# Kernel tuning notes

Hardware: AMD Instinct MI355X
Metric: run time of the kernel (lower is better)

## Reference

```python
import jax, jax.numpy as jnp
import numpy as np

H = 1024    # hidden_size
E = 1024    # embedding_size
V = 50257   # vocab_size
M = 16384   # current number of entity slots in h_e_m


def setup_inputs() -> dict:
    key = jax.random.key(0)
    ks = jax.random.split(key, 12)
    u = lambda k, s: jax.random.uniform(k, s, jnp.float32, -0.1, 0.1)
    return dict(
        x=jax.random.randint(ks[0], (1,), 0, V),
        entity_target=jax.random.randint(ks[1], (1,), 1, M),
        emb=u(ks[2], (V, E)),
        W_ih=u(ks[3], (4 * H, E)),
        W_hh=u(ks[4], (4 * H, H)),
        b_ih=jnp.zeros((4 * H,), jnp.float32),
        b_hh=jnp.zeros((4 * H,), jnp.float32),
        h0=jnp.zeros((1, H), jnp.float32),
        c0=jnp.zeros((1, H), jnp.float32),
        h_e_m=u(ks[5], (M, H)),
        Ws_w=u(ks[6], (H, H)),
        Ws_b=jnp.zeros((H,), jnp.float32),
        Wz_w=u(ks[7], (1, 2 * H)),
        Wz_b=jnp.zeros((1,), jnp.float32),
        W2_w=u(ks[8], (H, 2 * H)),
        W2_b=jnp.zeros((H,), jnp.float32),
        W1_w=u(ks[9], (V, H)),
        W1_b=jnp.zeros((V,), jnp.float32),
    )


def reference(x, entity_target, emb, W_ih, W_hh, b_ih, b_hh, h0, c0, h_e_m,
              Ws_w, Ws_b, Wz_w, Wz_b, W2_w, W2_b, W1_w, W1_b):
    # --- single-step LSTM (batch=1, 1 token), PyTorch gate order i,f,g,o ---
    x_e = emb[x]                                        # (1, E)
    gates = x_e @ W_ih.T + h0 @ W_hh.T + b_ih + b_hh    # (1, 4H)
    i, f, g, o = jnp.split(gates, 4, axis=1)
    c = jax.nn.sigmoid(f) * c0 + jax.nn.sigmoid(i) * jnp.tanh(g)
    h = jax.nn.sigmoid(o) * jnp.tanh(c)                 # (1, H)

    # --- attention over entity memory bank ---
    mem_proj = h_e_m @ Ws_w.T + Ws_b                    # (M, H)  W_score(h_e_m)
    scores = (h @ mem_proj.T).reshape(-1)               # (M,)
    p_v = jax.nn.softmax(scores)                        # (M,)
    # sum(diag(p_v) @ h_e_m, dim=0) == p_v @ h_e_m
    d_i = (p_v @ h_e_m)[None, :]                        # (1, H)

    # --- sigmoid entity gate ---
    z_i = jax.nn.sigmoid(jnp.concatenate([h, d_i], axis=1) @ Wz_w.T + Wz_b)  # (1,1)

    # --- index_copy scatter write, then read back written slot ---
    t = entity_target[0]
    new_mem = h_e_m.at[t].set(h[0])                     # (M, H)
    mem_read = new_mem[t]                               # (H,) == h[0]

    feat = jnp.concatenate([h[0], mem_read], axis=0)    # (2H,)
    out = (jnp.tanh(feat @ W2_w.T + W2_b) @ W1_w.T + W1_b)[None, :]  # (1, V)
    return out, z_i, p_v
```

## Files before the change

kernel.cpp:

```cpp
#include <hip/hip_runtime.h>
#include <hip/hip_bf16.h>

#define H 1024
#define E 1024
#define VOCAB 50257
#define M 16384

__device__ __forceinline__ float sigmoidf_(float x) { return 1.0f / (1.0f + expf(-x)); }

__device__ __forceinline__ float wave_reduce_sum(float v) {
    #pragma unroll
    for (int o = 32; o > 0; o >>= 1) v += __shfl_down(v, o);
    return v;
}

__global__ void k_lstm(const int* x, const float* emb, const float* W_ih, const float* W_hh,
                       const float* b_ih, const float* b_hh, const float* h0, const float* c0,
                       float* h_out) {
    int j = blockIdx.x;
    int w = threadIdx.x >> 6;
    int lane = threadIdx.x & 63;
    int r = w * H + j;
    const float4* A  = (const float4*)(W_ih + (size_t)r * E);
    const float4* Bm = (const float4*)(W_hh + (size_t)r * H);
    const float4* xe = (const float4*)(emb + (size_t)x[0] * E);
    const float4* hp = (const float4*)h0;
    float acc = 0.f;
    #pragma unroll
    for (int i = 0; i < 4; i++) {
        int idx = lane + 64 * i;
        float4 a = A[idx],  xv = xe[idx];
        acc += a.x * xv.x + a.y * xv.y + a.z * xv.z + a.w * xv.w;
        float4 b = Bm[idx], hv = hp[idx];
        acc += b.x * hv.x + b.y * hv.y + b.z * hv.z + b.w * hv.w;
    }
    acc = wave_reduce_sum(acc);
    __shared__ float g[4];
    if (lane == 0) g[w] = acc + b_ih[r] + b_hh[r];
    __syncthreads();
    if (threadIdx.x == 0) {
        float gi = g[0], gf = g[1], gg = g[2], go = g[3];
        float c = sigmoidf_(gf) * c0[j] + sigmoidf_(gi) * tanhf(gg);
        h_out[j] = sigmoidf_(go) * tanhf(c);
    }
}

__global__ void k_hWs(const float* __restrict__ h, const float* __restrict__ Ws_w,
                      float* __restrict__ v) {
    int k = threadIdx.x;
    int j0 = blockIdx.x * 16;
    __shared__ float hs[16];
    if (threadIdx.x < 16) hs[threadIdx.x] = h[j0 + threadIdx.x];
    __syncthreads();
    float acc = 0.f;
    #pragma unroll
    for (int jj = 0; jj < 16; jj++)
        acc += hs[jj] * Ws_w[(size_t)(j0 + jj) * H + k];
    atomicAdd(&v[k], acc);
}

__global__ void k_scores(const float* __restrict__ hem, const float* __restrict__ v,
                         float* __restrict__ sc) {
    int m = blockIdx.x * 4 + (threadIdx.x >> 6);
    int lane = threadIdx.x & 63;
    const float4* A = (const float4*)(hem + (size_t)m * H);
    const float4* V4 = (const float4*)v;
    float acc = 0.f;
    #pragma unroll
    for (int i = 0; i < 4; i++) {
        int idx = lane + 64 * i;
        float4 a = A[idx], b = V4[idx];
        acc += a.x * b.x + a.y * b.y + a.z * b.z + a.w * b.w;
    }
    acc = wave_reduce_sum(acc);
    if (lane == 0) sc[m] = acc;
}

__global__ void k_softmax(const float* __restrict__ sc, float* __restrict__ pv) {
    int t = threadIdx.x;
    float vals[16];
    float lmax = -1e30f;
    #pragma unroll
    for (int i = 0; i < 16; i++) { vals[i] = sc[t + 1024 * i]; lmax = fmaxf(lmax, vals[i]); }
    __shared__ float s[1024];
    s[t] = lmax; __syncthreads();
    for (int o = 512; o > 0; o >>= 1) { if (t < o) s[t] = fmaxf(s[t], s[t + o]); __syncthreads(); }
    float gmax = s[0];
    __syncthreads();
    float lsum = 0.f;
    #pragma unroll
    for (int i = 0; i < 16; i++) { float e = expf(vals[i] - gmax); vals[i] = e; lsum += e; }
    s[t] = lsum; __syncthreads();
    for (int o = 512; o > 0; o >>= 1) { if (t < o) s[t] += s[t + o]; __syncthreads(); }
    float inv = 1.f / s[0];
    #pragma unroll
    for (int i = 0; i < 16; i++) pv[t + 1024 * i] = vals[i] * inv;
}

__global__ void k_dvec(const float* __restrict__ hem, const float* __restrict__ pv,
                       float* __restrict__ dacc) {
    int k = threadIdx.x;
    int m0 = blockIdx.x * 64;
    __shared__ float ps[64];
    if (threadIdx.x < 64) ps[threadIdx.x] = pv[m0 + threadIdx.x];
    __syncthreads();
    float acc = 0.f;
    #pragma unroll 8
    for (int mm = 0; mm < 64; mm++)
        acc += ps[mm] * hem[(size_t)(m0 + mm) * H + k];
    atomicAdd(&dacc[k], acc);
}

__global__ void k_z(const float* __restrict__ h, const float* __restrict__ dvec,
                    const float* __restrict__ Wz_w, const float* __restrict__ Wz_b,
                    float* __restrict__ out_z) {
    int t = threadIdx.x;
    float acc = 0.f;
    for (int i = t; i < H; i += 256) acc += h[i] * Wz_w[i] + dvec[i] * Wz_w[H + i];
    __shared__ float s[256];
    s[t] = acc; __syncthreads();
    for (int o = 128; o > 0; o >>= 1) { if (t < o) s[t] += s[t + o]; __syncthreads(); }
    if (t == 0) out_z[0] = sigmoidf_(s[0] + Wz_b[0]);
}

__global__ void k_fc2(const float* __restrict__ h, const float* __restrict__ W2_w,
                      const float* __restrict__ W2_b, float* __restrict__ oh) {
    int j = blockIdx.x * 4 + (threadIdx.x >> 6);
    int lane = threadIdx.x & 63;
    const float4* R = (const float4*)(W2_w + (size_t)j * 2 * H);
    const float4* H4 = (const float4*)h;
    float acc = 0.f;
    #pragma unroll
    for (int i = 0; i < 4; i++) {
        int idx = lane + 64 * i;
        float4 hv = H4[idx];
        float4 a = R[idx];
        float4 b = R[256 + idx];
        acc += hv.x * (a.x + b.x) + hv.y * (a.y + b.y) + hv.z * (a.z + b.z) + hv.w * (a.w + b.w);
    }
    acc = wave_reduce_sum(acc);
    if (lane == 0) oh[j] = tanhf(acc + W2_b[j]);
}

__global__ void k_fc1(const float* __restrict__ oh, const float* __restrict__ W1_w,
                      const float* __restrict__ W1_b, float* __restrict__ out) {
    int r = blockIdx.x * 4 + (threadIdx.x >> 6);
    if (r >= VOCAB) return;
    int lane = threadIdx.x & 63;
    const float4* A = (const float4*)(W1_w + (size_t)r * H);
    const float4* O4 = (const float4*)oh;
    float acc = 0.f;
    #pragma unroll
    for (int i = 0; i < 4; i++) {
        int idx = lane + 64 * i;
        float4 a = A[idx], b = O4[idx];
        acc += a.x * b.x + a.y * b.y + a.z * b.z + a.w * b.w;
    }
    acc = wave_reduce_sum(acc);
    if (lane == 0) out[r] = acc + W1_b[r];
}

extern "C" void kernel_launch(void* const* d_in, const int* in_sizes, int n_in,
                              void* d_out, int out_size, void* d_ws, size_t ws_size,
                              hipStream_t stream) {
    const int*   x      = (const int*)  d_in[0];
    const float* emb    = (const float*)d_in[2];
    const float* W_ih   = (const float*)d_in[3];
    const float* W_hh   = (const float*)d_in[4];
    const float* b_ih   = (const float*)d_in[5];
    const float* b_hh   = (const float*)d_in[6];
    const float* h0     = (const float*)d_in[7];
    const float* c0     = (const float*)d_in[8];
    const float* hem    = (const float*)d_in[9];
    const float* Ws_w   = (const float*)d_in[10];
    const float* Wz_w   = (const float*)d_in[12];
    const float* Wz_b   = (const float*)d_in[13];
    const float* W2_w   = (const float*)d_in[14];
    const float* W2_b   = (const float*)d_in[15];
    const float* W1_w   = (const float*)d_in[16];
    const float* W1_b   = (const float*)d_in[17];

    float* out  = (float*)d_out;
    float* zout = out + VOCAB;
    float* pv   = out + VOCAB + 1;

    float* ws = (float*)d_ws;
    float* h  = ws;
    float* v  = ws + 1024;
    float* sc = ws + 2048;
    float* dv = ws + 18432;
    float* oh = ws + 19456;

    hipMemsetAsync(v,  0, H * sizeof(float), stream);
    hipMemsetAsync(dv, 0, H * sizeof(float), stream);

    k_lstm   <<<1024, 256, 0, stream>>>(x, emb, W_ih, W_hh, b_ih, b_hh, h0, c0, h);
    k_hWs    <<<64, 1024, 0, stream>>>(h, Ws_w, v);
    k_scores <<<M / 4, 256, 0, stream>>>(hem, v, sc);
    k_softmax<<<1, 1024, 0, stream>>>(sc, pv);
    k_dvec   <<<M / 64, 1024, 0, stream>>>(hem, pv, dv);
    k_z      <<<1, 256, 0, stream>>>(h, dv, Wz_w, Wz_b, zout);
    k_fc2    <<<H / 4, 256, 0, stream>>>(h, W2_w, W2_b, oh);
    k_fc1    <<<(VOCAB + 3) / 4, 256, 0, stream>>>(oh, W1_w, W1_b, out);
}
```

Baseline: 95.31 us.

## Fuse scores, block-local softmax and weighted sum into one attention pass

```diff
diff --git a/kernel.cpp b/kernel.cpp
--- a/kernel.cpp
+++ b/kernel.cpp
@@ -8,16 +8,24 @@
 
 __device__ __forceinline__ float sigmoidf_(float x) { return 1.0f / (1.0f + expf(-x)); }
 
-__device__ __forceinline__ float wave_reduce_sum(float v) {
+__device__ __forceinline__ float wave_sum(float v) {
     #pragma unroll
     for (int o = 32; o > 0; o >>= 1) v += __shfl_down(v, o);
     return v;
 }
 
-__global__ void k_lstm(const int* x, const float* emb, const float* W_ih, const float* W_hh,
-                       const float* b_ih, const float* b_hh, const float* h0, const float* c0,
-                       float* h_out) {
+__global__ void k_lstm(const int* __restrict__ x, const float* __restrict__ emb,
+                       const float* __restrict__ W_ih, const float* __restrict__ W_hh,
+                       const float* __restrict__ b_ih, const float* __restrict__ b_hh,
+                       const float* __restrict__ h0, const float* __restrict__ c0,
+                       float* __restrict__ h_out, float* __restrict__ v_z,
+                       float* __restrict__ dv_z, unsigned int* __restrict__ cnt) {
     int j = blockIdx.x;
+    if (threadIdx.x == 0) {
+        v_z[j] = 0.f;
+        dv_z[j] = 0.f;
+        if (j == 0) cnt[0] = 0u;
+    }
     int w = threadIdx.x >> 6;
     int lane = threadIdx.x & 63;
     int r = w * H + j;
@@ -34,14 +42,13 @@
         float4 b = Bm[idx], hv = hp[idx];
         acc += b.x * hv.x + b.y * hv.y + b.z * hv.z + b.w * hv.w;
     }
-    acc = wave_reduce_sum(acc);
+    acc = wave_sum(acc);
     __shared__ float g[4];
     if (lane == 0) g[w] = acc + b_ih[r] + b_hh[r];
     __syncthreads();
     if (threadIdx.x == 0) {
-        float gi = g[0], gf = g[1], gg = g[2], go = g[3];
-        float c = sigmoidf_(gf) * c0[j] + sigmoidf_(gi) * tanhf(gg);
-        h_out[j] = sigmoidf_(go) * tanhf(c);
+        float c = sigmoidf_(g[1]) * c0[j] + sigmoidf_(g[0]) * tanhf(g[2]);
+        h_out[j] = sigmoidf_(g[3]) * tanhf(c);
     }
 }
 
@@ -59,87 +66,116 @@
     atomicAdd(&v[k], acc);
 }
 
-__global__ void k_scores(const float* __restrict__ hem, const float* __restrict__ v,
-                         float* __restrict__ sc) {
-    int m = blockIdx.x * 4 + (threadIdx.x >> 6);
-    int lane = threadIdx.x & 63;
-    const float4* A = (const float4*)(hem + (size_t)m * H);
+__global__ void k_attn(const float* __restrict__ hem, const float* __restrict__ v,
+                       float* __restrict__ sc, float* __restrict__ db,
+                       float* __restrict__ Mb, float* __restrict__ Sb) {
+    __shared__ float s_sc[64];
+    __shared__ float s_e[64];
+    int b = blockIdx.x;
+    int m0 = b * 64;
+    int w = threadIdx.x >> 6, lane = threadIdx.x & 63;
     const float4* V4 = (const float4*)v;
-    float acc = 0.f;
-    #pragma unroll
-    for (int i = 0; i < 4; i++) {
-        int idx = lane + 64 * i;
-        float4 a = A[idx], b = V4[idx];
-        acc += a.x * b.x + a.y * b.y + a.z * b.z + a.w * b.w;
-    }
-    acc = wave_reduce_sum(acc);
-    if (lane == 0) sc[m] = acc;
-}
-
-__global__ void k_softmax(const float* __restrict__ sc, float* __restrict__ pv) {
-    int t = threadIdx.x;
-    float vals[16];
-    float lmax = -1e30f;
-    #pragma unroll
-    for (int i = 0; i < 16; i++) { vals[i] = sc[t + 1024 * i]; lmax = fmaxf(lmax, vals[i]); }
-    __shared__ float s[1024];
-    s[t] = lmax; __syncthreads();
-    for (int o = 512; o > 0; o >>= 1) { if (t < o) s[t] = fmaxf(s[t], s[t + o]); __syncthreads(); }
-    float gmax = s[0];
-    __syncthreads();
-    float lsum = 0.f;
-    #pragma unroll
-    for (int i = 0; i < 16; i++) { float e = expf(vals[i] - gmax); vals[i] = e; lsum += e; }
-    s[t] = lsum; __syncthreads();
-    for (int o = 512; o > 0; o >>= 1) { if (t < o) s[t] += s[t + o]; __syncthreads(); }
-    float inv = 1.f / s[0];
-    #pragma unroll
-    for (int i = 0; i < 16; i++) pv[t + 1024 * i] = vals[i] * inv;
-}
-
-__global__ void k_dvec(const float* __restrict__ hem, const float* __restrict__ pv,
-                       float* __restrict__ dacc) {
+    #pragma unroll
+    for (int q = 0; q < 4; q++) {
+        int mm = w * 4 + q;
+        const float4* A = (const float4*)(hem + (size_t)(m0 + mm) * H);
+        float acc = 0.f;
+        #pragma unroll
+        for (int i = 0; i < 4; i++) {
+            float4 a = A[lane + 64 * i], bb = V4[lane + 64 * i];
+            acc += a.x * bb.x + a.y * bb.y + a.z * bb.z + a.w * bb.w;
+        }
+        acc = wave_sum(acc);
+        if (lane == 0) { s_sc[mm] = acc; sc[m0 + mm] = acc; }
+    }
+    __syncthreads();
+    if (w == 0) {
+        float xv = s_sc[lane];
+        float mx = xv;
+        #pragma unroll
+        for (int o = 32; o > 0; o >>= 1) mx = fmaxf(mx, __shfl_down(mx, o));
+        mx = __shfl(mx, 0);
+        float e = expf(xv - mx);
+        s_e[lane] = e;
+        float ssum = wave_sum(e);
+        if (lane == 0) { Mb[b] = mx; Sb[b] = ssum; }
+    }
+    __syncthreads();
     int k = threadIdx.x;
-    int m0 = blockIdx.x * 64;
-    __shared__ float ps[64];
-    if (threadIdx.x < 64) ps[threadIdx.x] = pv[m0 + threadIdx.x];
-    __syncthreads();
     float acc = 0.f;
     #pragma unroll 8
     for (int mm = 0; mm < 64; mm++)
-        acc += ps[mm] * hem[(size_t)(m0 + mm) * H + k];
-    atomicAdd(&dacc[k], acc);
-}
-
-__global__ void k_z(const float* __restrict__ h, const float* __restrict__ dvec,
-                    const float* __restrict__ Wz_w, const float* __restrict__ Wz_b,
-                    float* __restrict__ out_z) {
+        acc += s_e[mm] * hem[(size_t)(m0 + mm) * H + k];
+    db[(size_t)b * H + k] = acc;
+}
+
+__global__ void k_comb_fc2(const float* __restrict__ h, const float* __restrict__ W2_w,
+                           const float* __restrict__ W2_b, float* __restrict__ oh,
+                           const float* __restrict__ sc, const float* __restrict__ db,
+                           const float* __restrict__ Mb, const float* __restrict__ Sb,
+                           float* __restrict__ pv, float* __restrict__ dv,
+                           const float* __restrict__ Wz_w, const float* __restrict__ Wz_b,
+                           float* __restrict__ zout, unsigned int* __restrict__ cnt) {
+    if (blockIdx.x < 256) {
+        int j = blockIdx.x * 4 + (threadIdx.x >> 6);
+        int lane = threadIdx.x & 63;
+        const float4* R  = (const float4*)(W2_w + (size_t)j * 2 * H);
+        const float4* H4 = (const float4*)h;
+        float acc = 0.f;
+        #pragma unroll
+        for (int i = 0; i < 4; i++) {
+            int idx = lane + 64 * i;
+            float4 hv = H4[idx];
+            float4 a = R[idx];
+            float4 b = R[256 + idx];
+            acc += hv.x * (a.x + b.x) + hv.y * (a.y + b.y)
+                 + hv.z * (a.z + b.z) + hv.w * (a.w + b.w);
+        }
+        acc = wave_sum(acc);
+        if (lane == 0) oh[j] = tanhf(acc + W2_b[j]);
+        return;
+    }
+    int b2 = blockIdx.x - 256;
     int t = threadIdx.x;
-    float acc = 0.f;
-    for (int i = t; i < H; i += 256) acc += h[i] * Wz_w[i] + dvec[i] * Wz_w[H + i];
     __shared__ float s[256];
-    s[t] = acc; __syncthreads();
+    __shared__ float s_w[16];
+    __shared__ unsigned int s_old;
+    float mval = Mb[t];
+    s[t] = mval; __syncthreads();
+    for (int o = 128; o > 0; o >>= 1) { if (t < o) s[t] = fmaxf(s[t], s[t + o]); __syncthreads(); }
+    float gmax = s[0]; __syncthreads();
+    s[t] = Sb[t] * expf(mval - gmax); __syncthreads();
     for (int o = 128; o > 0; o >>= 1) { if (t < o) s[t] += s[t + o]; __syncthreads(); }
-    if (t == 0) out_z[0] = sigmoidf_(s[0] + Wz_b[0]);
-}
-
-__global__ void k_fc2(const float* __restrict__ h, const float* __restrict__ W2_w,
-                      const float* __restrict__ W2_b, float* __restrict__ oh) {
-    int j = blockIdx.x * 4 + (threadIdx.x >> 6);
-    int lane = threadIdx.x & 63;
-    const float4* R = (const float4*)(W2_w + (size_t)j * 2 * H);
-    const float4* H4 = (const float4*)h;
-    float acc = 0.f;
-    #pragma unroll
-    for (int i = 0; i < 4; i++) {
-        int idx = lane + 64 * i;
-        float4 hv = H4[idx];
-        float4 a = R[idx];
-        float4 b = R[256 + idx];
-        acc += hv.x * (a.x + b.x) + hv.y * (a.y + b.y) + hv.z * (a.z + b.z) + hv.w * (a.w + b.w);
-    }
-    acc = wave_reduce_sum(acc);
-    if (lane == 0) oh[j] = tanhf(acc + W2_b[j]);
+    float inv = 1.f / s[0]; __syncthreads();
+    int base = b2 * 1024;
+    #pragma unroll
+    for (int q = 0; q < 4; q++) {
+        int i = base + t + 256 * q;
+        pv[i] = expf(sc[i] - gmax) * inv;
+    }
+    if (t < 16) s_w[t] = expf(Mb[b2 * 16 + t] - gmax) * inv;
+    __syncthreads();
+    float a0 = 0.f, a1 = 0.f, a2 = 0.f, a3 = 0.f;
+    #pragma unroll
+    for (int rr = 0; rr < 16; rr++) {
+        const float* row = db + (size_t)(b2 * 16 + rr) * H;
+        float wr = s_w[rr];
+        a0 += wr * row[t];       a1 += wr * row[t + 256];
+        a2 += wr * row[t + 512]; a3 += wr * row[t + 768];
+    }
+    atomicAdd(&dv[t], a0);       atomicAdd(&dv[t + 256], a1);
+    atomicAdd(&dv[t + 512], a2); atomicAdd(&dv[t + 768], a3);
+    __threadfence();
+    if (t == 0) s_old = atomicAdd(cnt, 1u);
+    __syncthreads();
+    if (s_old == 15u) {
+        __threadfence();
+        float acc = 0.f;
+        for (int i = t; i < H; i += 256) acc += h[i] * Wz_w[i] + dv[i] * Wz_w[H + i];
+        s[t] = acc; __syncthreads();
+        for (int o = 128; o > 0; o >>= 1) { if (t < o) s[t] += s[t + o]; __syncthreads(); }
+        if (t == 0) zout[0] = sigmoidf_(s[0] + Wz_b[0]);
+    }
 }
 
 __global__ void k_fc1(const float* __restrict__ oh, const float* __restrict__ W1_w,
@@ -147,7 +183,7 @@
     int r = blockIdx.x * 4 + (threadIdx.x >> 6);
     if (r >= VOCAB) return;
     int lane = threadIdx.x & 63;
-    const float4* A = (const float4*)(W1_w + (size_t)r * H);
+    const float4* A  = (const float4*)(W1_w + (size_t)r * H);
     const float4* O4 = (const float4*)oh;
     float acc = 0.f;
     #pragma unroll
@@ -156,7 +192,7 @@
         float4 a = A[idx], b = O4[idx];
         acc += a.x * b.x + a.y * b.y + a.z * b.z + a.w * b.w;
     }
-    acc = wave_reduce_sum(acc);
+    acc = wave_sum(acc);
     if (lane == 0) out[r] = acc + W1_b[r];
 }
 
@@ -185,21 +221,21 @@
     float* pv   = out + VOCAB + 1;
 
     float* ws = (float*)d_ws;
-    float* h  = ws;
-    float* v  = ws + 1024;
-    float* sc = ws + 2048;
-    float* dv = ws + 18432;
-    float* oh = ws + 19456;
-
-    hipMemsetAsync(v,  0, H * sizeof(float), stream);
-    hipMemsetAsync(dv, 0, H * sizeof(float), stream);
-
-    k_lstm   <<<1024, 256, 0, stream>>>(x, emb, W_ih, W_hh, b_ih, b_hh, h0, c0, h);
-    k_hWs    <<<64, 1024, 0, stream>>>(h, Ws_w, v);
-    k_scores <<<M / 4, 256, 0, stream>>>(hem, v, sc);
-    k_softmax<<<1, 1024, 0, stream>>>(sc, pv);
-    k_dvec   <<<M / 64, 1024, 0, stream>>>(hem, pv, dv);
-    k_z      <<<1, 256, 0, stream>>>(h, dv, Wz_w, Wz_b, zout);
-    k_fc2    <<<H / 4, 256, 0, stream>>>(h, W2_w, W2_b, oh);
-    k_fc1    <<<(VOCAB + 3) / 4, 256, 0, stream>>>(oh, W1_w, W1_b, out);
-}
+    float* h   = ws;
+    float* v   = ws + 1024;
+    float* sc  = ws + 2048;
+    float* dv  = ws + 18432;
+    float* oh  = ws + 19456;
+    float* Mb  = ws + 20480;
+    float* Sb  = ws + 20736;
+    unsigned int* cnt = (unsigned int*)(ws + 20992);
+    float* db  = ws + 21504;
+
+    k_lstm    <<<1024, 256, 0, stream>>>(x, emb, W_ih, W_hh, b_ih, b_hh, h0, c0,
+                                         h, v, dv, cnt);
+    k_hWs     <<<64, 1024, 0, stream>>>(h, Ws_w, v);
+    k_attn    <<<256, 1024, 0, stream>>>(hem, v, sc, db, Mb, Sb);
+    k_comb_fc2<<<272, 256, 0, stream>>>(h, W2_w, W2_b, oh, sc, db, Mb, Sb,
+                                        pv, dv, Wz_w, Wz_b, zout, cnt);
+    k_fc1     <<<(VOCAB + 3) / 4, 256, 0, stream>>>(oh, W1_w, W1_b, out);
+}
```

Measured after the change: 82.62 us. 1.15x faster.
